# Kernel optimization log

Hardware: AMD Instinct MI355X
Metric: run time of the kernel (lower is better)

Reference implementation:

```python
import jax, jax.numpy as jnp
import numpy as np
from jax import lax

D_MODEL = 1024
N_EXPERTS = 8
N_ACTIVE = 2
FFN_HIDDEN = int(D_MODEL * 2.0)


def setup_inputs() -> dict:
    key = jax.random.key(0)
    ks = jax.random.split(key, 7)
    B, T = 2, 2048
    s_in = 1.0 / np.sqrt(D_MODEL)
    s_h = 1.0 / np.sqrt(FFN_HIDDEN)
    return {
        "x": jax.random.normal(ks[0], (B, T, D_MODEL), dtype=jnp.float32),
        # router: torch Linear(d_model, n_experts, bias=False) weight [E, D]
        "router_w": jax.random.uniform(ks[1], (N_EXPERTS, D_MODEL), jnp.float32, -s_in, s_in),
        # stacked expert FFN params: w1 [E, H, D], b1 [E, H], w2 [E, D, H], b2 [E, D]
        "w1": jax.random.uniform(ks[2], (N_EXPERTS, FFN_HIDDEN, D_MODEL), jnp.float32, -s_in, s_in),
        "b1": jax.random.uniform(ks[3], (N_EXPERTS, FFN_HIDDEN), jnp.float32, -s_in, s_in),
        "w2": jax.random.uniform(ks[4], (N_EXPERTS, D_MODEL, FFN_HIDDEN), jnp.float32, -s_h, s_h),
        "b2": jax.random.uniform(ks[5], (N_EXPERTS, D_MODEL), jnp.float32, -s_h, s_h),
    }


def reference(x, router_w, w1, b1, w2, b2):
    B, T, D = x.shape
    N = B * T
    xf = x.reshape(N, D)

    logits = xf @ router_w.T                      # [N, E]
    probs = jax.nn.softmax(logits, axis=-1)       # [N, E]

    # --- aux load-balancing loss (f_i is non-differentiable, from indices) ---
    _, disp_idx = lax.top_k(logits, N_ACTIVE)     # [N, K]
    disp_mask = jax.nn.one_hot(disp_idx, N_EXPERTS, dtype=logits.dtype).sum(axis=1)  # [N, E]
    f_i = disp_mask.sum(axis=0) / (N * N_ACTIVE)  # [E]
    P_i = probs.mean(axis=0)                      # [E]
    aux_loss = N_EXPERTS * jnp.sum(f_i * P_i)

    # --- top-k combine weights, renormalized ---
    topk_w, topk_idx = lax.top_k(probs, N_ACTIVE)                 # [N, K]
    topk_w = topk_w / topk_w.sum(axis=-1, keepdims=True)
    # scatter top-k weights into dense [N, E] combine matrix (zeros elsewhere)
    combine_w = (jax.nn.one_hot(topk_idx, N_EXPERTS, dtype=xf.dtype) * topk_w[..., None]).sum(axis=1)

    # --- expert FFNs, weighted combine (loop over small fixed expert set) ---
    out = jnp.zeros_like(xf)
    for e in range(N_EXPERTS):
        h = jax.nn.silu(xf @ w1[e].T + b1[e])     # [N, H]
        y = h @ w2[e].T + b2[e]                   # [N, D]
        out = out + combine_w[:, e:e + 1] * y

    return out.reshape(B, T, D), aux_loss
```

## Files before the change

kernel.cpp:

```cpp
#include <hip/hip_runtime.h>
#include <cstdint>
#include <cstddef>

#define D_MODEL 1024
#define N_EXPERTS 8
#define FFN_H 2048
#define N_TOK 4096
#define CAP 2048

typedef float f32x4 __attribute__((ext_vector_type(4)));
typedef __bf16 bf16x8 __attribute__((ext_vector_type(8)));

static constexpr size_t XB_OFF   = 0;
static constexpr size_t W1B_OFF  = XB_OFF  + (size_t)N_TOK * D_MODEL * 2;
static constexpr size_t W2B_OFF  = W1B_OFF + (size_t)N_EXPERTS * FFN_H * D_MODEL * 2;
static constexpr size_t HBUF_OFF = W2B_OFF + (size_t)N_EXPERTS * D_MODEL * FFN_H * 2;
static constexpr size_t YBUF_OFF = HBUF_OFF + (size_t)N_EXPERTS * CAP * FFN_H * 2;
static constexpr size_t CNT_OFF  = YBUF_OFF + (size_t)N_EXPERTS * CAP * D_MODEL * 2;
static constexpr size_t PSUM_OFF = CNT_OFF + 32;
static constexpr size_t TOK_OFF  = PSUM_OFF + 32;
static constexpr size_t TIX_OFF  = TOK_OFF + (size_t)N_EXPERTS * CAP * 4;
static constexpr size_t TIW_OFF  = TIX_OFF + (size_t)N_TOK * 8;

__device__ __forceinline__ void async_ld16(const void* g, void* l) {
    __builtin_amdgcn_global_load_lds(
        (const __attribute__((address_space(1))) unsigned int*)g,
        (__attribute__((address_space(3))) unsigned int*)l, 16, 0, 0);
}

__global__ __launch_bounds__(256) void prep_kernel(const float* __restrict__ x,
                                                   const float* __restrict__ rw,
                                                   const float* __restrict__ w1,
                                                   const float* __restrict__ w2,
                                                   __bf16* __restrict__ xb,
                                                   __bf16* __restrict__ w1b,
                                                   __bf16* __restrict__ w2b,
                                                   int* __restrict__ counts,
                                                   float* __restrict__ psum,
                                                   int* __restrict__ tok_list,
                                                   int2* __restrict__ tinfo_idx,
                                                   float2* __restrict__ tinfo_w) {
    __shared__ float rws[N_EXPERTS * D_MODEL];
    __shared__ int s_e0[64], s_e1[64], s_r0[64], s_r1[64];
    __shared__ float s_w0[64], s_w1[64];
    __shared__ int hist[8], base[8];
    __shared__ float pacc[8];

    int tid = threadIdx.x;
    int b = blockIdx.x;
    if (b >= 64) {
        int c = b - 64;
        const float* src; __bf16* dst; size_t bb;
        if (c < 2048)       { src = x;  dst = xb;  bb = (size_t)c * 2048; }
        else if (c < 10240) { src = w1; dst = w1b; bb = (size_t)(c - 2048) * 2048; }
        else                { src = w2; dst = w2b; bb = (size_t)(c - 10240) * 2048; }
        size_t i = bb + (size_t)tid * 8;
        float4 a = *reinterpret_cast<const float4*>(src + i);
        float4 d = *reinterpret_cast<const float4*>(src + i + 4);
        bf16x8 r;
        r[0] = (__bf16)a.x; r[1] = (__bf16)a.y; r[2] = (__bf16)a.z; r[3] = (__bf16)a.w;
        r[4] = (__bf16)d.x; r[5] = (__bf16)d.y; r[6] = (__bf16)d.z; r[7] = (__bf16)d.w;
        *reinterpret_cast<bf16x8*>(dst + i) = r;
        return;
    }

    for (int i = tid * 4; i < N_EXPERTS * D_MODEL; i += 256 * 4)
        *reinterpret_cast<float4*>(&rws[i]) = *reinterpret_cast<const float4*>(&rw[i]);
    if (tid < 8) { hist[tid] = 0; pacc[tid] = 0.f; }
    __syncthreads();

    int wave = tid >> 6, lane = tid & 63;
    float psacc[8] = {};
    for (int it = 0; it < 16; ++it) {
        int li = wave * 16 + it;
        int t = b * 64 + li;
        const float* xr = x + (size_t)t * D_MODEL;
        float acc[8] = {};
#pragma unroll
        for (int i = 0; i < D_MODEL / 64; ++i) {
            float xv = xr[lane + 64 * i];
#pragma unroll
            for (int e = 0; e < 8; ++e) acc[e] += xv * rws[e * D_MODEL + lane + 64 * i];
        }
        float logit[8];
#pragma unroll
        for (int e = 0; e < 8; ++e) {
            float v = acc[e];
            for (int off = 32; off; off >>= 1) v += __shfl_xor(v, off);
            logit[e] = v;
        }
        float mx = logit[0];
#pragma unroll
        for (int e = 1; e < 8; ++e) mx = fmaxf(mx, logit[e]);
        float p[8], s = 0.f;
#pragma unroll
        for (int e = 0; e < 8; ++e) { p[e] = expf(logit[e] - mx); s += p[e]; }
        float inv = 1.f / s;
#pragma unroll
        for (int e = 0; e < 8; ++e) { p[e] *= inv; psacc[e] += p[e]; }
        int e0 = 0; float p0 = p[0];
#pragma unroll
        for (int e = 1; e < 8; ++e) if (p[e] > p0) { p0 = p[e]; e0 = e; }
        int e1 = -1; float p1 = -1.f;
#pragma unroll
        for (int e = 0; e < 8; ++e) if (e != e0 && p[e] > p1) { p1 = p[e]; e1 = e; }
        float invw = 1.f / (p0 + p1);
        if (lane == 0) {
            s_e0[li] = e0; s_e1[li] = e1;
            s_w0[li] = p0 * invw; s_w1[li] = p1 * invw;
        }
    }
    if (lane == 0)
#pragma unroll
        for (int e = 0; e < 8; ++e) atomicAdd(&pacc[e], psacc[e]);
    __syncthreads();

    if (tid < 64) {
        s_r0[tid] = atomicAdd(&hist[s_e0[tid]], 1);
        s_r1[tid] = atomicAdd(&hist[s_e1[tid]], 1);
    }
    __syncthreads();
    if (tid < 8) {
        base[tid] = atomicAdd(&counts[tid], hist[tid]);
        atomicAdd(&psum[tid], pacc[tid]);
    }
    __syncthreads();
    if (tid < 64) {
        int t = b * 64 + tid;
        int e0 = s_e0[tid], e1 = s_e1[tid];
        int q0 = min(base[e0] + s_r0[tid], CAP - 1);
        int q1 = min(base[e1] + s_r1[tid], CAP - 1);
        tok_list[e0 * CAP + q0] = t;
        tok_list[e1 * CAP + q1] = t;
        tinfo_idx[t] = make_int2(e0 * CAP + q0, e1 * CAP + q1);
        tinfo_w[t] = make_float2(s_w0[tid], s_w1[tid]);
    }
}

template <int KDIM, bool PASS2>
__global__ __launch_bounds__(256, 4) void ffn_kernel(const __bf16* __restrict__ A_base,
                                                     const __bf16* __restrict__ B_base,
                                                     const float* __restrict__ bias,
                                                     const int* __restrict__ counts,
                                                     const int* __restrict__ tok_list,
                                                     __bf16* __restrict__ Out_base) {
    constexpr int BROWS = PASS2 ? D_MODEL : FFN_H;
    constexpr int NT = BROWS / 128;
    int bid = blockIdx.x;
    int e = bid & 7;
    int r = bid >> 3;
    int n0 = (r % NT) * 128;
    int m0 = (r / NT) * 128;
    int cnt = min(counts[e], CAP);
    if (m0 >= cnt) return;

    __shared__ __bf16 s_a[2][128 * 32];
    __shared__ __bf16 s_b[2][128 * 32];
    __shared__ int s_tok[128];

    int tid = threadIdx.x;
    if (!PASS2 && tid < 128) {
        int slot = min(m0 + tid, cnt - 1);
        s_tok[tid] = tok_list[e * CAP + slot];
    }
    __syncthreads();

    int colk = (tid & 3) * 8;
    const __bf16 *a_src0, *a_src1;
    if (PASS2) {
        int s0 = min(m0 + (tid >> 2), cnt - 1);
        int s1 = min(m0 + 64 + (tid >> 2), cnt - 1);
        a_src0 = A_base + ((size_t)e * CAP + s0) * KDIM + colk;
        a_src1 = A_base + ((size_t)e * CAP + s1) * KDIM + colk;
    } else {
        a_src0 = A_base + (size_t)s_tok[tid >> 2] * KDIM + colk;
        a_src1 = A_base + (size_t)s_tok[64 + (tid >> 2)] * KDIM + colk;
    }
    const __bf16* b_src0 = B_base + ((size_t)e * BROWS + n0 + (tid >> 2)) * KDIM + colk;
    const __bf16* b_src1 = b_src0 + (size_t)64 * KDIM;

    char* lds_a = (char*)&s_a[0][0] + (tid >> 6) * 1024;
    char* lds_b = (char*)&s_b[0][0] + (tid >> 6) * 1024;

    int wv = tid >> 6, lane = tid & 63;
    int wm = wv >> 1, wn = wv & 1;
    int lm = lane & 15, q = lane >> 4;
    int a_base = (wm * 64 + lm) * 32 + q * 8;
    int b_base = (wn * 64 + lm) * 32 + q * 8;

    f32x4 acc[4][4] = {};
    for (int k0 = 0; k0 < KDIM; k0 += 64) {
        async_ld16(a_src0 + k0,      lds_a);
        async_ld16(a_src1 + k0,      lds_a + 4096);
        async_ld16(a_src0 + k0 + 32, lds_a + 8192);
        async_ld16(a_src1 + k0 + 32, lds_a + 8192 + 4096);
        async_ld16(b_src0 + k0,      lds_b);
        async_ld16(b_src1 + k0,      lds_b + 4096);
        async_ld16(b_src0 + k0 + 32, lds_b + 8192);
        async_ld16(b_src1 + k0 + 32, lds_b + 8192 + 4096);
        __syncthreads();
#pragma unroll
        for (int kk = 0; kk < 2; ++kk) {
            bf16x8 af[4], bf[4];
#pragma unroll
            for (int f = 0; f < 4; ++f) {
                af[f] = *reinterpret_cast<const bf16x8*>(&s_a[kk][a_base + f * 16 * 32]);
                bf[f] = *reinterpret_cast<const bf16x8*>(&s_b[kk][b_base + f * 16 * 32]);
            }
#pragma unroll
            for (int fm = 0; fm < 4; ++fm)
#pragma unroll
                for (int fn = 0; fn < 4; ++fn)
                    acc[fm][fn] = __builtin_amdgcn_mfma_f32_16x16x32_bf16(af[fm], bf[fn], acc[fm][fn], 0, 0, 0);
        }
        __syncthreads();
    }

#pragma unroll
    for (int fn = 0; fn < 4; ++fn) {
        int n = n0 + wn * 64 + fn * 16 + lm;
        float bv = bias[e * BROWS + n];
#pragma unroll
        for (int fm = 0; fm < 4; ++fm) {
            int rbase = wm * 64 + fm * 16 + q * 4;
#pragma unroll
            for (int i = 0; i < 4; ++i) {
                int row = rbase + i;
                int slot = m0 + row;
                if (slot < cnt) {
                    float v = acc[fm][fn][i] + bv;
                    if (!PASS2) {
                        float sv = v / (1.f + __expf(-v));
                        Out_base[((size_t)e * CAP + slot) * FFN_H + n] = (__bf16)sv;
                    } else {
                        Out_base[((size_t)e * CAP + slot) * D_MODEL + n] = (__bf16)v;
                    }
                }
            }
        }
    }
}

__global__ __launch_bounds__(256) void combine_kernel(const __bf16* __restrict__ ybuf,
                                                      const int2* __restrict__ tinfo_idx,
                                                      const float2* __restrict__ tinfo_w,
                                                      const int* __restrict__ counts,
                                                      const float* __restrict__ psum,
                                                      float* __restrict__ out) {
    int tid = threadIdx.x;
    if (blockIdx.x == 0 && tid == 0) {
        float s = 0.f;
#pragma unroll
        for (int e = 0; e < 8; ++e)
            s += ((float)counts[e] / (float)(N_TOK * 2)) * (psum[e] / (float)N_TOK);
        out[(size_t)N_TOK * D_MODEL] = 8.f * s;
    }
    int t = blockIdx.x * 2 + (tid >> 7);
    int d0 = (tid & 127) * 8;
    int2 ix = tinfo_idx[t];
    float2 w = tinfo_w[t];
    bf16x8 ya = *reinterpret_cast<const bf16x8*>(ybuf + (size_t)ix.x * D_MODEL + d0);
    bf16x8 yb = *reinterpret_cast<const bf16x8*>(ybuf + (size_t)ix.y * D_MODEL + d0);
    float4 o0, o1;
    o0.x = w.x * (float)ya[0] + w.y * (float)yb[0];
    o0.y = w.x * (float)ya[1] + w.y * (float)yb[1];
    o0.z = w.x * (float)ya[2] + w.y * (float)yb[2];
    o0.w = w.x * (float)ya[3] + w.y * (float)yb[3];
    o1.x = w.x * (float)ya[4] + w.y * (float)yb[4];
    o1.y = w.x * (float)ya[5] + w.y * (float)yb[5];
    o1.z = w.x * (float)ya[6] + w.y * (float)yb[6];
    o1.w = w.x * (float)ya[7] + w.y * (float)yb[7];
    float* op = out + (size_t)t * D_MODEL + d0;
    *reinterpret_cast<float4*>(op) = o0;
    *reinterpret_cast<float4*>(op + 4) = o1;
}

extern "C" void kernel_launch(void* const* d_in, const int* in_sizes, int n_in,
                              void* d_out, int out_size, void* d_ws, size_t ws_size,
                              hipStream_t stream) {
    const float* x  = (const float*)d_in[0];
    const float* rw = (const float*)d_in[1];
    const float* w1 = (const float*)d_in[2];
    const float* b1 = (const float*)d_in[3];
    const float* w2 = (const float*)d_in[4];
    const float* b2 = (const float*)d_in[5];
    float* out = (float*)d_out;

    char* ws = (char*)d_ws;
    __bf16* xb     = (__bf16*)(ws + XB_OFF);
    __bf16* w1b    = (__bf16*)(ws + W1B_OFF);
    __bf16* w2b    = (__bf16*)(ws + W2B_OFF);
    __bf16* hbuf   = (__bf16*)(ws + HBUF_OFF);
    __bf16* ybuf   = (__bf16*)(ws + YBUF_OFF);
    int*    counts = (int*)(ws + CNT_OFF);
    float*  psum   = (float*)(ws + PSUM_OFF);
    int*    tok    = (int*)(ws + TOK_OFF);
    int2*   tix    = (int2*)(ws + TIX_OFF);
    float2* tiw    = (float2*)(ws + TIW_OFF);

    hipMemsetAsync(ws + CNT_OFF, 0, 64, stream);

    prep_kernel<<<64 + 18432, 256, 0, stream>>>(x, rw, w1, w2, xb, w1b, w2b,
                                                counts, psum, tok, tix, tiw);

    ffn_kernel<D_MODEL, false><<<8 * (FFN_H / 128) * (CAP / 128), 256, 0, stream>>>(
        xb, w1b, b1, counts, tok, hbuf);
    ffn_kernel<FFN_H, true><<<8 * (D_MODEL / 128) * (CAP / 128), 256, 0, stream>>>(
        hbuf, w2b, b2, counts, tok, ybuf);

    combine_kernel<<<N_TOK / 2, 256, 0, stream>>>(ybuf, tix, tiw, counts, psum, out);
}
```

Measured before the change: 308.2 us.

## Double-buffer FFN GEMM K-loop, swizzle LDS layout, stage epilogue through LDS

The FFN GEMM kernel now prefetches the next K-step tile into a second LDS buffer while running MFMAs on the current one, which removes one barrier per iteration and overlaps global loads with compute. The LDS column layout is XOR-swizzled, with the same swizzle applied to the global source offsets, to avoid bank conflicts on the fragment reads. The epilogue writes results to LDS first and then stores 16-byte vectors to global memory instead of scattered 2-byte stores. LDS use grows to 64KB per block and the occupancy hint drops from 4 to 2 blocks per CU.

Measured after the change: 293.5 us. -4.8%, faster.

```diff
diff --git a/kernel.cpp b/kernel.cpp
--- a/kernel.cpp
+++ b/kernel.cpp
@@ -138,7 +138,7 @@
 }
 
 template <int KDIM, bool PASS2>
-__global__ __launch_bounds__(256, 4) void ffn_kernel(const __bf16* __restrict__ A_base,
+__global__ __launch_bounds__(256, 2) void ffn_kernel(const __bf16* __restrict__ A_base,
                                                      const __bf16* __restrict__ B_base,
                                                      const float* __restrict__ bias,
                                                      const int* __restrict__ counts,
@@ -146,6 +146,7 @@
                                                      __bf16* __restrict__ Out_base) {
     constexpr int BROWS = PASS2 ? D_MODEL : FFN_H;
     constexpr int NT = BROWS / 128;
+    constexpr int NSTEP = KDIM / 64;
     int bid = blockIdx.x;
     int e = bid & 7;
     int r = bid >> 3;
@@ -154,18 +155,17 @@
     int cnt = min(counts[e], CAP);
     if (m0 >= cnt) return;
 
-    __shared__ __bf16 s_a[2][128 * 32];
-    __shared__ __bf16 s_b[2][128 * 32];
-    __shared__ int s_tok[128];
+    __shared__ char smem[65536];
 
     int tid = threadIdx.x;
+    int* s_tok = (int*)smem;
     if (!PASS2 && tid < 128) {
         int slot = min(m0 + tid, cnt - 1);
         s_tok[tid] = tok_list[e * CAP + slot];
     }
     __syncthreads();
 
-    int colk = (tid & 3) * 8;
+    int colk = ((tid & 3) ^ ((tid >> 3) & 3)) * 8;
     const __bf16 *a_src0, *a_src1;
     if (PASS2) {
         int s0 = min(m0 + (tid >> 2), cnt - 1);
@@ -178,66 +178,84 @@
     }
     const __bf16* b_src0 = B_base + ((size_t)e * BROWS + n0 + (tid >> 2)) * KDIM + colk;
     const __bf16* b_src1 = b_src0 + (size_t)64 * KDIM;
-
-    char* lds_a = (char*)&s_a[0][0] + (tid >> 6) * 1024;
-    char* lds_b = (char*)&s_b[0][0] + (tid >> 6) * 1024;
+    __syncthreads();
 
     int wv = tid >> 6, lane = tid & 63;
     int wm = wv >> 1, wn = wv & 1;
     int lm = lane & 15, q = lane >> 4;
-    int a_base = (wm * 64 + lm) * 32 + q * 8;
-    int b_base = (wn * 64 + lm) * 32 + q * 8;
+    int rsw = ((q ^ ((lm >> 1) & 3)) * 8);
+    int a_base = (wm * 64 + lm) * 32 + rsw;
+    int b_base = (wn * 64 + lm) * 32 + rsw;
+
+    char* wofs_a = smem + (tid >> 6) * 1024;
+    char* wofs_b = smem + 32768 + (tid >> 6) * 1024;
 
     f32x4 acc[4][4] = {};
-    for (int k0 = 0; k0 < KDIM; k0 += 64) {
-        async_ld16(a_src0 + k0,      lds_a);
-        async_ld16(a_src1 + k0,      lds_a + 4096);
-        async_ld16(a_src0 + k0 + 32, lds_a + 8192);
-        async_ld16(a_src1 + k0 + 32, lds_a + 8192 + 4096);
-        async_ld16(b_src0 + k0,      lds_b);
-        async_ld16(b_src1 + k0,      lds_b + 4096);
-        async_ld16(b_src0 + k0 + 32, lds_b + 8192);
-        async_ld16(b_src1 + k0 + 32, lds_b + 8192 + 4096);
+
+    {
+        char* la = wofs_a; char* lb = wofs_b;
+        async_ld16(a_src0,      la);        async_ld16(a_src1,      la + 4096);
+        async_ld16(a_src0 + 32, la + 8192); async_ld16(a_src1 + 32, la + 8192 + 4096);
+        async_ld16(b_src0,      lb);        async_ld16(b_src1,      lb + 4096);
+        async_ld16(b_src0 + 32, lb + 8192); async_ld16(b_src1 + 32, lb + 8192 + 4096);
+    }
+    __syncthreads();
+
+    int cur = 0;
+    for (int t = 0; t < NSTEP; ++t) {
+        if (t + 1 < NSTEP) {
+            int k0 = (t + 1) * 64;
+            char* la = wofs_a + ((cur ^ 1) * 16384);
+            char* lb = wofs_b + ((cur ^ 1) * 16384);
+            async_ld16(a_src0 + k0,      la);        async_ld16(a_src1 + k0,      la + 4096);
+            async_ld16(a_src0 + k0 + 32, la + 8192); async_ld16(a_src1 + k0 + 32, la + 8192 + 4096);
+            async_ld16(b_src0 + k0,      lb);        async_ld16(b_src1 + k0,      lb + 4096);
+            async_ld16(b_src0 + k0 + 32, lb + 8192); async_ld16(b_src1 + k0 + 32, lb + 8192 + 4096);
+        }
+#pragma unroll
+        for (int kk = 0; kk < 2; ++kk) {
+            const __bf16* pa = (const __bf16*)(smem + (cur * 2 + kk) * 8192);
+            const __bf16* pb = (const __bf16*)(smem + 32768 + (cur * 2 + kk) * 8192);
+            bf16x8 af[4], bfg[4];
+#pragma unroll
+            for (int f = 0; f < 4; ++f) {
+                af[f]  = *reinterpret_cast<const bf16x8*>(&pa[a_base + f * 16 * 32]);
+                bfg[f] = *reinterpret_cast<const bf16x8*>(&pb[b_base + f * 16 * 32]);
+            }
+#pragma unroll
+            for (int fm = 0; fm < 4; ++fm)
+#pragma unroll
+                for (int fn = 0; fn < 4; ++fn)
+                    acc[fm][fn] = __builtin_amdgcn_mfma_f32_16x16x32_bf16(af[fm], bfg[fn], acc[fm][fn], 0, 0, 0);
+        }
         __syncthreads();
-#pragma unroll
-        for (int kk = 0; kk < 2; ++kk) {
-            bf16x8 af[4], bf[4];
-#pragma unroll
-            for (int f = 0; f < 4; ++f) {
-                af[f] = *reinterpret_cast<const bf16x8*>(&s_a[kk][a_base + f * 16 * 32]);
-                bf[f] = *reinterpret_cast<const bf16x8*>(&s_b[kk][b_base + f * 16 * 32]);
-            }
-#pragma unroll
-            for (int fm = 0; fm < 4; ++fm)
-#pragma unroll
-                for (int fn = 0; fn < 4; ++fn)
-                    acc[fm][fn] = __builtin_amdgcn_mfma_f32_16x16x32_bf16(af[fm], bf[fn], acc[fm][fn], 0, 0, 0);
-        }
-        __syncthreads();
-    }
-
+        cur ^= 1;
+    }
+
+    __bf16* ep = (__bf16*)(smem) + wv * (64 * 72);
 #pragma unroll
     for (int fn = 0; fn < 4; ++fn) {
         int n = n0 + wn * 64 + fn * 16 + lm;
         float bv = bias[e * BROWS + n];
 #pragma unroll
-        for (int fm = 0; fm < 4; ++fm) {
-            int rbase = wm * 64 + fm * 16 + q * 4;
+        for (int fm = 0; fm < 4; ++fm)
 #pragma unroll
             for (int i = 0; i < 4; ++i) {
-                int row = rbase + i;
-                int slot = m0 + row;
-                if (slot < cnt) {
-                    float v = acc[fm][fn][i] + bv;
-                    if (!PASS2) {
-                        float sv = v / (1.f + __expf(-v));
-                        Out_base[((size_t)e * CAP + slot) * FFN_H + n] = (__bf16)sv;
-                    } else {
-                        Out_base[((size_t)e * CAP + slot) * D_MODEL + n] = (__bf16)v;
-                    }
-                }
+                float v = acc[fm][fn][i] + bv;
+                if (!PASS2) v = v / (1.f + __expf(-v));
+                ep[(fm * 16 + q * 4 + i) * 72 + fn * 16 + lm] = (__bf16)v;
             }
-        }
+    }
+    __syncthreads();
+    int rr = lane >> 3, ccol = (lane & 7) * 8;
+#pragma unroll
+    for (int rep = 0; rep < 8; ++rep) {
+        int rw = rep * 8 + rr;
+        int slot = m0 + wm * 64 + rw;
+        bf16x8 vv = *reinterpret_cast<const bf16x8*>(&ep[rw * 72 + ccol]);
+        if (slot < cnt)
+            *reinterpret_cast<bf16x8*>(
+                &Out_base[((size_t)e * CAP + slot) * BROWS + n0 + wn * 64 + ccol]) = vv;
     }
 }
 
```
